# Optimization experiments

Hardware: AMD Instinct MI355X
Metric: run time of the kernel (lower is better)

The kernel has to match this reference:

```python
import jax, jax.numpy as jnp
import numpy as np

D_MODEL = 1024
N_HEADS = 16
N_MEM = 64
D_K = D_MODEL // N_HEADS


def setup_inputs() -> dict:
    key = jax.random.key(0)
    ks = jax.random.split(key, 16)
    B, N = 2, 2048
    s = 1.0 / np.sqrt(D_MODEL)  # xavier-ish scale
    inp = {
        "q": jax.random.normal(ks[0], (B, N, D_MODEL), jnp.float32),
        "k": jax.random.normal(ks[1], (B, N, D_MODEL), jnp.float32),
        "v": jax.random.normal(ks[2], (B, N, D_MODEL), jnp.float32),
        "attention_mask": jax.random.randint(ks[3], (B, 1, 1, N), 0, 2).astype(bool),
        "Wq": jax.random.normal(ks[4], (D_MODEL, D_MODEL), jnp.float32) * s,
        "bq": jnp.zeros((D_MODEL,), jnp.float32),
        "Wk": jax.random.normal(ks[5], (D_MODEL, D_MODEL), jnp.float32) * s,
        "bk": jnp.zeros((D_MODEL,), jnp.float32),
        "Wv": jax.random.normal(ks[6], (D_MODEL, D_MODEL), jnp.float32) * s,
        "bv": jnp.zeros((D_MODEL,), jnp.float32),
        "Wo": jax.random.normal(ks[7], (D_MODEL, D_MODEL), jnp.float32) * s,
        "bo": jnp.zeros((D_MODEL,), jnp.float32),
        "m_k": jax.random.normal(ks[8], (1, N_MEM, D_MODEL), jnp.float32) * 0.01,
        "m_v": jax.random.normal(ks[9], (1, N_MEM, D_MODEL), jnp.float32) * 0.01,
    }
    return inp


def reference(q, k, v, attention_mask, Wq, bq, Wk, bk, Wv, bv, Wo, bo, m_k, m_v):
    B, Nq, D = q.shape
    nk = k.shape[1]
    H, dk, M = N_HEADS, D_K, N_MEM

    # projections (torch Linear: x @ W.T + b)
    qh = (q @ Wq.T + bq).reshape(B, Nq, H, dk).transpose(0, 2, 1, 3)  # b h nq d
    k_proj = k @ Wk.T + bk                                            # b nk d_model
    v_proj = v @ Wv.T + bv

    # append scaled memory slots along key/value length
    mk = jnp.broadcast_to(m_k * np.sqrt(dk), (B, M, D))
    mv = jnp.broadcast_to(m_v * np.sqrt(M), (B, M, D))
    kk = jnp.concatenate([k_proj, mk], axis=1)                        # b (nk+M) d_model
    vv = jnp.concatenate([v_proj, mv], axis=1)

    kh = kk.reshape(B, nk + M, H, dk).transpose(0, 2, 1, 3)          # b h nkM d
    vh = vv.reshape(B, nk + M, H, dk).transpose(0, 2, 1, 3)

    scores = jnp.einsum('bhqd,bhkd->bhqk', qh, kh) / np.sqrt(dk)      # b h nq (nk+M)

    # mask applies only to the first nk key positions; memory slots unmasked
    pad_mask = jnp.concatenate(
        [jnp.broadcast_to(attention_mask, (B, 1, 1, nk)),
         jnp.zeros((B, 1, 1, M), bool)], axis=-1)
    scores = jnp.where(pad_mask, -jnp.inf, scores)

    p_attn = jax.nn.softmax(scores, axis=-1)  # dropout p=0.0 -> identity
    out = jnp.einsum('bhqk,bhkd->bhqd', p_attn, vh)
    out = out.transpose(0, 2, 1, 3).reshape(B, Nq, D)
    return out @ Wo.T + bo
```

## Files before the change

### kernel.cpp

```cpp
#include <hip/hip_runtime.h>
#include <hip/hip_bf16.h>

typedef __attribute__((ext_vector_type(8))) short bf16x8;
typedef __attribute__((ext_vector_type(4))) float f32x4;

__device__ __forceinline__ short f2b(float x) {
    __hip_bfloat16 h = __float2bfloat16(x);
    short s;
    __builtin_memcpy(&s, &h, 2);
    return s;
}

__device__ __forceinline__ void gload16(const short* g, const short* l) {
    __builtin_amdgcn_global_load_lds((const __attribute__((address_space(1))) void*)g,
                                     (__attribute__((address_space(3))) void*)l, 16, 0, 0);
}

__global__ __launch_bounds__(256) void k_prep(const float* __restrict__ q,
                                              const float* __restrict__ k,
                                              const float* __restrict__ v,
                                              const float* __restrict__ Wq,
                                              const float* __restrict__ Wk,
                                              const float* __restrict__ Wv,
                                              const float* __restrict__ Wo,
                                              const float* __restrict__ mk,
                                              const float* __restrict__ mv,
                                              short* __restrict__ dst,
                                              short* __restrict__ kcat,
                                              short* __restrict__ vcat,
                                              short* __restrict__ vt) {
    const int y = blockIdx.y;
    const int i0 = blockIdx.x * 256 + threadIdx.x;
    if (y < 3) {
        const float* src = (y == 0) ? q : (y == 1) ? k : v;
        size_t base = (size_t)y * 1048576;
        #pragma unroll
        for (int it = 0; it < 4; ++it) {
            int off = i0 + it * 262144;
            float4 val = ((const float4*)src)[off];
            short4 o;
            o.x = f2b(val.x); o.y = f2b(val.y); o.z = f2b(val.z); o.w = f2b(val.w);
            ((short4*)dst)[base + off] = o;
        }
    } else if (y < 7) {
        const float* src = (y == 3) ? Wq : (y == 4) ? Wk : (y == 5) ? Wv : Wo;
        size_t base = 3145728 + (size_t)(y - 3) * 262144;
        float4 val = ((const float4*)src)[i0];
        short4 o;
        o.x = f2b(val.x); o.y = f2b(val.y); o.z = f2b(val.z); o.w = f2b(val.w);
        ((short4*)dst)[base + i0] = o;
    } else {
        if (i0 < 131072) {
            int b = i0 >> 16;
            int r = (i0 >> 10) & 63;
            int d = i0 & 1023;
            kcat[((size_t)(b * 2176 + 2048 + r)) * 1024 + d] = f2b(mk[r * 1024 + d] * 8.0f);
            vcat[((size_t)(b * 2176 + 2048 + r)) * 1024 + d] = f2b(mv[r * 1024 + d] * 8.0f);
            kcat[((size_t)(b * 2176 + 2112 + r)) * 1024 + d] = 0;
            int h = (i0 >> 12) & 15, dd = (i0 >> 6) & 63, c = i0 & 63;
            vt[((size_t)((b * 16 + h) * 64 + dd)) * 2176 + 2112 + c] = 0;
        }
    }
}

template <int MODE>
__device__ __forceinline__ void gemm_core(const short* __restrict__ A,
                                          const short* __restrict__ Bw,
                                          const float* __restrict__ bias,
                                          void* __restrict__ Cout,
                                          int bm, int bn,
                                          short (*As)[32], short (*Bs)[32]) {
    const int tid = threadIdx.x;
    const int w = tid >> 6, lane = tid & 63;
    const int wm = w >> 1, wn = w & 1;
    const int lr = lane & 15, lg = lane >> 4;
    const int rseg = lane >> 2;
    const int c_src = (lane & 3) ^ ((lane >> 3) & 3);
    const int slot = lg ^ ((lr >> 1) & 3);

    const short* Ab = A + (size_t)(bm * 128) * 1024;
    const short* Bb = Bw + (size_t)(bn * 128) * 1024;

    f32x4 acc[4][4] = {};

    for (int k0 = 0; k0 < 1024; k0 += 32) {
        __syncthreads();
        #pragma unroll
        for (int jj = 0; jj < 2; ++jj) {
            int seg = w * 2 + jj;
            int row = seg * 16 + rseg;
            gload16(Ab + (size_t)row * 1024 + k0 + c_src * 8, &As[seg * 16][0]);
            gload16(Bb + (size_t)row * 1024 + k0 + c_src * 8, &Bs[seg * 16][0]);
        }
        __syncthreads();
        bf16x8 af[4], bfr[4];
        #pragma unroll
        for (int m = 0; m < 4; ++m) {
            int row = wm * 64 + m * 16 + lr;
            af[m] = *(const bf16x8*)((const char*)As + row * 64 + slot * 16);
        }
        #pragma unroll
        for (int n = 0; n < 4; ++n) {
            int row = wn * 64 + n * 16 + lr;
            bfr[n] = *(const bf16x8*)((const char*)Bs + row * 64 + slot * 16);
        }
        #pragma unroll
        for (int m = 0; m < 4; ++m)
            #pragma unroll
            for (int n = 0; n < 4; ++n)
                acc[m][n] = __builtin_amdgcn_mfma_f32_16x16x32_bf16(af[m], bfr[n], acc[m][n], 0, 0, 0);
    }

    #pragma unroll
    for (int m = 0; m < 4; ++m) {
        #pragma unroll
        for (int n = 0; n < 4; ++n) {
            int col = bn * 128 + wn * 64 + n * 16 + lr;
            float bv = bias[col];
            #pragma unroll
            for (int r = 0; r < 4; ++r) {
                int row = bm * 128 + wm * 64 + m * 16 + lg * 4 + r;
                float val = acc[m][n][r] + bv;
                if (MODE == 0) {
                    ((short*)Cout)[(size_t)row * 1024 + col] = f2b(val);
                } else if (MODE == 1) {
                    int rr = (row >> 11) * 2176 + (row & 2047);
                    ((short*)Cout)[(size_t)rr * 1024 + col] = f2b(val);
                } else {
                    ((float*)Cout)[(size_t)row * 1024 + col] = val;
                }
            }
        }
    }
}

__global__ __launch_bounds__(256) void k_gemm_qkv(const short* __restrict__ qb,
                                                  const short* __restrict__ kb,
                                                  const short* __restrict__ vb,
                                                  const short* __restrict__ Wqb,
                                                  const short* __restrict__ Wkb,
                                                  const short* __restrict__ Wvb,
                                                  const float* __restrict__ bq,
                                                  const float* __restrict__ bk,
                                                  const float* __restrict__ bv,
                                                  short* __restrict__ qp,
                                                  short* __restrict__ kcat,
                                                  short* __restrict__ vcat) {
    __shared__ __align__(16) short As[128][32];
    __shared__ __align__(16) short Bs[128][32];
    const int z = blockIdx.z;
    if (z == 0)      gemm_core<0>(qb, Wqb, bq, qp,   blockIdx.x, blockIdx.y, As, Bs);
    else if (z == 1) gemm_core<1>(kb, Wkb, bk, kcat, blockIdx.x, blockIdx.y, As, Bs);
    else             gemm_core<1>(vb, Wvb, bv, vcat, blockIdx.x, blockIdx.y, As, Bs);
}

__global__ __launch_bounds__(256) void k_gemm_o(const short* __restrict__ aout,
                                                const short* __restrict__ Wob,
                                                const float* __restrict__ bo,
                                                float* __restrict__ out) {
    __shared__ __align__(16) short As[128][32];
    __shared__ __align__(16) short Bs[128][32];
    gemm_core<2>(aout, Wob, bo, out, blockIdx.x, blockIdx.y, As, Bs);
}

__global__ __launch_bounds__(256) void k_vtrans(const short* __restrict__ vcat,
                                                short* __restrict__ vt) {
    __shared__ __align__(16) short t[64][72];
    const int kk0 = blockIdx.x * 64, h = blockIdx.y, b = blockIdx.z;
    const int tid = threadIdx.x;
    const int r = tid >> 3, c = tid & 7;
    #pragma unroll
    for (int i = 0; i < 2; ++i) {
        int row = r + i * 32;
        bf16x8 v = *(const bf16x8*)(vcat + ((size_t)(b * 2176 + kk0 + row)) * 1024 + h * 64 + c * 8);
        *(bf16x8*)(&t[row][c * 8]) = v;
    }
    __syncthreads();
    #pragma unroll
    for (int i = 0; i < 2; ++i) {
        int d = r + i * 32;
        bf16x8 outv;
        #pragma unroll
        for (int j = 0; j < 8; ++j) outv[j] = t[c * 8 + j][d];
        *(bf16x8*)(vt + ((size_t)((b * 16 + h) * 64 + d)) * 2176 + kk0 + c * 8) = outv;
    }
}

__global__ __launch_bounds__(256) void k_attn(const short* __restrict__ qp,
                                              const short* __restrict__ kcat,
                                              const short* __restrict__ vt,
                                              const int* __restrict__ maskI,
                                              short* __restrict__ aout) {
    __shared__ __align__(16) short Ks[2][64][64];
    __shared__ __align__(16) short Vs[2][64][64];
    __shared__ __align__(16) short Pt[4][32][72];
    __shared__ float smask[2176];

    const int bid = blockIdx.x;
    const int x = bid & 7, j = bid >> 3;
    const int g = x + 8 * (j & 3);
    const int qt = j >> 2;
    const int h = g & 15, b = g >> 4;

    const int tid = threadIdx.x;
    const int w = tid >> 6, lane = tid & 63;
    const int lr = lane & 15, lg = lane >> 4;

    for (int i = tid; i < 2176; i += 256) {
        float mval;
        if (i < 2048) mval = maskI[b * 2048 + i] ? -INFINITY : 0.0f;
        else          mval = 0.0f;
        smask[i] = mval;
    }

    const short* Kb = kcat + (size_t)b * 2176 * 1024 + h * 64;
    const short* Vb = vt + ((size_t)(b * 16 + h) * 64) * 2176;

    const int srow8 = lane >> 3;
    const int schunk = (lane & 7) ^ srow8;

    #pragma unroll
    for (int jj = 0; jj < 2; ++jj) {
        int seg = w * 2 + jj;
        int row = seg * 8 + srow8;
        gload16(Kb + (size_t)row * 1024 + schunk * 8, &Ks[0][seg * 8][0]);
        gload16(Vb + (size_t)row * 2176 + schunk * 8, &Vs[0][seg * 8][0]);
    }

    const size_t qbase = ((size_t)(b * 2048 + qt * 128 + w * 32)) * 1024 + h * 64;
    bf16x8 qf[2][2];
    #pragma unroll
    for (int m = 0; m < 2; ++m)
        #pragma unroll
        for (int ks = 0; ks < 2; ++ks)
            qf[m][ks] = *(const bf16x8*)(qp + qbase + (size_t)(m * 16 + lr) * 1024 + ks * 32 + lg * 8);

    float m_run[2][4], l_part[2][4];
    f32x4 o[2][4] = {};
    #pragma unroll
    for (int m = 0; m < 2; ++m)
        #pragma unroll
        for (int r = 0; r < 4; ++r) { m_run[m][r] = -1e30f; l_part[m][r] = 0.0f; }

    __syncthreads();

    int cur = 0;
    for (int t = 0; t < 33; ++t) {
        const int key0 = t * 64;

        if (t < 32) {
            const int nk0 = key0 + 64;
            #pragma unroll
            for (int jj = 0; jj < 2; ++jj) {
                int seg = w * 2 + jj;
                int row = seg * 8 + srow8;
                gload16(Kb + (size_t)(nk0 + row) * 1024 + schunk * 8, &Ks[cur ^ 1][seg * 8][0]);
                gload16(Vb + (size_t)row * 2176 + nk0 + schunk * 8, &Vs[cur ^ 1][seg * 8][0]);
            }
        }

        f32x4 s[2][4] = {};
        #pragma unroll
        for (int ks = 0; ks < 2; ++ks)
            #pragma unroll
            for (int n = 0; n < 4; ++n) {
                int krow = n * 16 + lr;
                int kchunk = (ks * 4 + lg) ^ (lr & 7);
                bf16x8 kf = *(const bf16x8*)((const char*)(&Ks[cur][0][0]) + krow * 128 + kchunk * 16);
                s[0][n] = __builtin_amdgcn_mfma_f32_16x16x32_bf16(qf[0][ks], kf, s[0][n], 0, 0, 0);
                s[1][n] = __builtin_amdgcn_mfma_f32_16x16x32_bf16(qf[1][ks], kf, s[1][n], 0, 0, 0);
            }

        float madd[4];
        #pragma unroll
        for (int n = 0; n < 4; ++n) madd[n] = smask[key0 + n * 16 + lr];

        float lmax[2][4];
        float dmax = -1e30f;
        #pragma unroll
        for (int m = 0; m < 2; ++m)
            #pragma unroll
            for (int r = 0; r < 4; ++r) {
                float a0 = s[m][0][r] * 0.125f + madd[0];
                float a1 = s[m][1][r] * 0.125f + madd[1];
                float a2 = s[m][2][r] * 0.125f + madd[2];
                float a3 = s[m][3][r] * 0.125f + madd[3];
                s[m][0][r] = a0; s[m][1][r] = a1; s[m][2][r] = a2; s[m][3][r] = a3;
                float lm = fmaxf(fmaxf(a0, a1), fmaxf(a2, a3));
                lmax[m][r] = lm;
                dmax = fmaxf(dmax, lm - m_run[m][r]);
            }

        if (__any(dmax > 3.0f)) {
            #pragma unroll
            for (int m = 0; m < 2; ++m)
                #pragma unroll
                for (int r = 0; r < 4; ++r) {
                    float tm = lmax[m][r];
                    #pragma unroll
                    for (int off = 1; off < 16; off <<= 1) tm = fmaxf(tm, __shfl_xor(tm, off));
                    float mnew = fmaxf(m_run[m][r], tm);
                    float corr = __expf(m_run[m][r] - mnew);
                    m_run[m][r] = mnew;
                    l_part[m][r] *= corr;
                    #pragma unroll
                    for (int nO = 0; nO < 4; ++nO) o[m][nO][r] *= corr;
                }
        }

        #pragma unroll
        for (int m = 0; m < 2; ++m)
            #pragma unroll
            for (int n = 0; n < 4; ++n)
                #pragma unroll
                for (int r = 0; r < 4; ++r) {
                    float p = __expf(s[m][n][r] - m_run[m][r]);
                    l_part[m][r] += p;
                    Pt[w][m * 16 + lg * 4 + r][n * 16 + lr] = f2b(p);
                }

        #pragma unroll
        for (int ks2 = 0; ks2 < 2; ++ks2) {
            bf16x8 pa[2];
            pa[0] = *(const bf16x8*)(&Pt[w][lr][ks2 * 32 + lg * 8]);
            pa[1] = *(const bf16x8*)(&Pt[w][16 + lr][ks2 * 32 + lg * 8]);
            #pragma unroll
            for (int nO = 0; nO < 4; ++nO) {
                int vrow = nO * 16 + lr;
                int vchunk = (ks2 * 4 + lg) ^ (lr & 7);
                bf16x8 vf = *(const bf16x8*)((const char*)(&Vs[cur][0][0]) + vrow * 128 + vchunk * 16);
                o[0][nO] = __builtin_amdgcn_mfma_f32_16x16x32_bf16(pa[0], vf, o[0][nO], 0, 0, 0);
                o[1][nO] = __builtin_amdgcn_mfma_f32_16x16x32_bf16(pa[1], vf, o[1][nO], 0, 0, 0);
            }
        }

        __syncthreads();
        cur ^= 1;
    }

    #pragma unroll
    for (int m = 0; m < 2; ++m) {
        #pragma unroll
        for (int r = 0; r < 4; ++r) {
            float l = l_part[m][r];
            #pragma unroll
            for (int off = 1; off < 16; off <<= 1) l += __shfl_xor(l, off);
            float inv = 1.0f / l;
            int qrow = qt * 128 + w * 32 + m * 16 + lg * 4 + r;
            #pragma unroll
            for (int nO = 0; nO < 4; ++nO)
                aout[((size_t)(b * 2048 + qrow)) * 1024 + h * 64 + nO * 16 + lr] =
                    f2b(o[m][nO][r] * inv);
        }
    }
}

extern "C" void kernel_launch(void* const* d_in, const int* in_sizes, int n_in,
                              void* d_out, int out_size, void* d_ws, size_t ws_size,
                              hipStream_t stream) {
    const float* q  = (const float*)d_in[0];
    const float* k  = (const float*)d_in[1];
    const float* v  = (const float*)d_in[2];
    const int* mask = (const int*)d_in[3];
    const float* Wq = (const float*)d_in[4];
    const float* bq = (const float*)d_in[5];
    const float* Wk = (const float*)d_in[6];
    const float* bk = (const float*)d_in[7];
    const float* Wv = (const float*)d_in[8];
    const float* bv = (const float*)d_in[9];
    const float* Wo = (const float*)d_in[10];
    const float* bo = (const float*)d_in[11];
    const float* mk = (const float*)d_in[12];
    const float* mv = (const float*)d_in[13];

    char* ws = (char*)d_ws;
    size_t off = 0;
    auto alloc = [&](size_t bytes) {
        char* p = ws + off;
        off += (bytes + 255) & ~(size_t)255;
        return p;
    };
    short* qb   = (short*)alloc(4096ull * 1024 * 2);
    short* kb   = (short*)alloc(4096ull * 1024 * 2);
    short* vb   = (short*)alloc(4096ull * 1024 * 2);
    short* Wqb  = (short*)alloc(1024ull * 1024 * 2);
    short* Wkb  = (short*)alloc(1024ull * 1024 * 2);
    short* Wvb  = (short*)alloc(1024ull * 1024 * 2);
    short* Wob  = (short*)alloc(1024ull * 1024 * 2);
    short* qp   = (short*)alloc(4096ull * 1024 * 2);
    short* kcat = (short*)alloc(2ull * 2176 * 1024 * 2);
    short* vcat = (short*)alloc(2ull * 2176 * 1024 * 2);
    short* vtb  = (short*)alloc(2ull * 16 * 64 * 2176 * 2);
    short* aout = (short*)alloc(4096ull * 1024 * 2);

    k_prep<<<dim3(1024, 8), 256, 0, stream>>>(q, k, v, Wq, Wk, Wv, Wo, mk, mv,
                                              qb, kcat, vcat, vtb);

    k_gemm_qkv<<<dim3(32, 8, 3), 256, 0, stream>>>(qb, kb, vb, Wqb, Wkb, Wvb,
                                                   bq, bk, bv, qp, kcat, vcat);

    k_vtrans<<<dim3(33, 16, 2), 256, 0, stream>>>(vcat, vtb);

    k_attn<<<512, 256, 0, stream>>>(qp, kcat, vtb, mask, aout);

    k_gemm_o<<<dim3(32, 8), 256, 0, stream>>>(aout, Wob, bo, (float*)d_out);
}
```

Before: 153.6 us.

## Use 8 waves of 16 query rows and transposed S=K·Q MFMA layout in attention

Doubles the attention block to 512 threads so each wave handles 16 query rows instead of 32. The score MFMA operands are swapped so each lane holds one query column, which removes the 16-lane max and sum shuffle reductions and vectorizes the mask load. P is written to LDS as packed pairs, and an explicit lgkmcnt wait is added before P is read back. This halves per-wave register pressure and should raise parallelism, but each K/V tile is now amortized over fewer rows per wave and the per-row correction needs extra lane shuffles.

```diff
diff --git a/kernel.cpp b/kernel.cpp
--- a/kernel.cpp
+++ b/kernel.cpp
@@ -186,14 +186,14 @@
     }
 }
 
-__global__ __launch_bounds__(256) void k_attn(const short* __restrict__ qp,
+__global__ __launch_bounds__(512) void k_attn(const short* __restrict__ qp,
                                               const short* __restrict__ kcat,
                                               const short* __restrict__ vt,
                                               const int* __restrict__ maskI,
                                               short* __restrict__ aout) {
     __shared__ __align__(16) short Ks[2][64][64];
     __shared__ __align__(16) short Vs[2][64][64];
-    __shared__ __align__(16) short Pt[4][32][72];
+    __shared__ __align__(16) short Pt[8][16][72];
     __shared__ float smask[2176];
 
     const int bid = blockIdx.x;
@@ -206,7 +206,7 @@
     const int w = tid >> 6, lane = tid & 63;
     const int lr = lane & 15, lg = lane >> 4;
 
-    for (int i = tid; i < 2176; i += 256) {
+    for (int i = tid; i < 2176; i += 512) {
         float mval;
         if (i < 2048) mval = maskI[b * 2048 + i] ? -INFINITY : 0.0f;
         else          mval = 0.0f;
@@ -219,28 +219,20 @@
     const int srow8 = lane >> 3;
     const int schunk = (lane & 7) ^ srow8;
 
-    #pragma unroll
-    for (int jj = 0; jj < 2; ++jj) {
-        int seg = w * 2 + jj;
-        int row = seg * 8 + srow8;
-        gload16(Kb + (size_t)row * 1024 + schunk * 8, &Ks[0][seg * 8][0]);
-        gload16(Vb + (size_t)row * 2176 + schunk * 8, &Vs[0][seg * 8][0]);
-    }
-
-    const size_t qbase = ((size_t)(b * 2048 + qt * 128 + w * 32)) * 1024 + h * 64;
-    bf16x8 qf[2][2];
-    #pragma unroll
-    for (int m = 0; m < 2; ++m)
-        #pragma unroll
-        for (int ks = 0; ks < 2; ++ks)
-            qf[m][ks] = *(const bf16x8*)(qp + qbase + (size_t)(m * 16 + lr) * 1024 + ks * 32 + lg * 8);
-
-    float m_run[2][4], l_part[2][4];
-    f32x4 o[2][4] = {};
-    #pragma unroll
-    for (int m = 0; m < 2; ++m)
-        #pragma unroll
-        for (int r = 0; r < 4; ++r) { m_run[m][r] = -1e30f; l_part[m][r] = 0.0f; }
+    {
+        int row = w * 8 + srow8;
+        gload16(Kb + (size_t)row * 1024 + schunk * 8, &Ks[0][w * 8][0]);
+        gload16(Vb + (size_t)row * 2176 + schunk * 8, &Vs[0][w * 8][0]);
+    }
+
+    const size_t qbase = ((size_t)(b * 2048 + qt * 128 + w * 16)) * 1024 + h * 64;
+    bf16x8 qf[2];
+    #pragma unroll
+    for (int ks = 0; ks < 2; ++ks)
+        qf[ks] = *(const bf16x8*)(qp + qbase + (size_t)lr * 1024 + ks * 32 + lg * 8);
+
+    float m_run = -1e30f, l_part = 0.0f;
+    f32x4 o[4] = {};
 
     __syncthreads();
 
@@ -250,16 +242,12 @@
 
         if (t < 32) {
             const int nk0 = key0 + 64;
-            #pragma unroll
-            for (int jj = 0; jj < 2; ++jj) {
-                int seg = w * 2 + jj;
-                int row = seg * 8 + srow8;
-                gload16(Kb + (size_t)(nk0 + row) * 1024 + schunk * 8, &Ks[cur ^ 1][seg * 8][0]);
-                gload16(Vb + (size_t)row * 2176 + nk0 + schunk * 8, &Vs[cur ^ 1][seg * 8][0]);
-            }
-        }
-
-        f32x4 s[2][4] = {};
+            int row = w * 8 + srow8;
+            gload16(Kb + (size_t)(nk0 + row) * 1024 + schunk * 8, &Ks[cur ^ 1][w * 8][0]);
+            gload16(Vb + (size_t)row * 2176 + nk0 + schunk * 8, &Vs[cur ^ 1][w * 8][0]);
+        }
+
+        f32x4 s[4] = {};
         #pragma unroll
         for (int ks = 0; ks < 2; ++ks)
             #pragma unroll
@@ -267,70 +255,62 @@
                 int krow = n * 16 + lr;
                 int kchunk = (ks * 4 + lg) ^ (lr & 7);
                 bf16x8 kf = *(const bf16x8*)((const char*)(&Ks[cur][0][0]) + krow * 128 + kchunk * 16);
-                s[0][n] = __builtin_amdgcn_mfma_f32_16x16x32_bf16(qf[0][ks], kf, s[0][n], 0, 0, 0);
-                s[1][n] = __builtin_amdgcn_mfma_f32_16x16x32_bf16(qf[1][ks], kf, s[1][n], 0, 0, 0);
+                s[n] = __builtin_amdgcn_mfma_f32_16x16x32_bf16(kf, qf[ks], s[n], 0, 0, 0);
             }
 
-        float madd[4];
-        #pragma unroll
-        for (int n = 0; n < 4; ++n) madd[n] = smask[key0 + n * 16 + lr];
-
-        float lmax[2][4];
-        float dmax = -1e30f;
-        #pragma unroll
-        for (int m = 0; m < 2; ++m)
+        float lm = -1e30f;
+        #pragma unroll
+        for (int n = 0; n < 4; ++n) {
+            float4 mq = *(const float4*)(&smask[key0 + n * 16 + lg * 4]);
+            s[n][0] = s[n][0] * 0.125f + mq.x;
+            s[n][1] = s[n][1] * 0.125f + mq.y;
+            s[n][2] = s[n][2] * 0.125f + mq.z;
+            s[n][3] = s[n][3] * 0.125f + mq.w;
+            lm = fmaxf(lm, fmaxf(fmaxf(s[n][0], s[n][1]), fmaxf(s[n][2], s[n][3])));
+        }
+
+        if (__any(lm - m_run > 3.0f)) {
+            float tm = lm;
+            tm = fmaxf(tm, __shfl_xor(tm, 16));
+            tm = fmaxf(tm, __shfl_xor(tm, 32));
+            float mnew = fmaxf(m_run, tm);
+            float corr = __expf(m_run - mnew);
+            m_run = mnew;
+            l_part *= corr;
             #pragma unroll
             for (int r = 0; r < 4; ++r) {
-                float a0 = s[m][0][r] * 0.125f + madd[0];
-                float a1 = s[m][1][r] * 0.125f + madd[1];
-                float a2 = s[m][2][r] * 0.125f + madd[2];
-                float a3 = s[m][3][r] * 0.125f + madd[3];
-                s[m][0][r] = a0; s[m][1][r] = a1; s[m][2][r] = a2; s[m][3][r] = a3;
-                float lm = fmaxf(fmaxf(a0, a1), fmaxf(a2, a3));
-                lmax[m][r] = lm;
-                dmax = fmaxf(dmax, lm - m_run[m][r]);
+                float cb = __shfl(corr, 20 * lg + r);
+                #pragma unroll
+                for (int nO = 0; nO < 4; ++nO) o[nO][r] *= cb;
             }
-
-        if (__any(dmax > 3.0f)) {
-            #pragma unroll
-            for (int m = 0; m < 2; ++m)
-                #pragma unroll
-                for (int r = 0; r < 4; ++r) {
-                    float tm = lmax[m][r];
-                    #pragma unroll
-                    for (int off = 1; off < 16; off <<= 1) tm = fmaxf(tm, __shfl_xor(tm, off));
-                    float mnew = fmaxf(m_run[m][r], tm);
-                    float corr = __expf(m_run[m][r] - mnew);
-                    m_run[m][r] = mnew;
-                    l_part[m][r] *= corr;
-                    #pragma unroll
-                    for (int nO = 0; nO < 4; ++nO) o[m][nO][r] *= corr;
-                }
-        }
-
-        #pragma unroll
-        for (int m = 0; m < 2; ++m)
-            #pragma unroll
-            for (int n = 0; n < 4; ++n)
-                #pragma unroll
-                for (int r = 0; r < 4; ++r) {
-                    float p = __expf(s[m][n][r] - m_run[m][r]);
-                    l_part[m][r] += p;
-                    Pt[w][m * 16 + lg * 4 + r][n * 16 + lr] = f2b(p);
-                }
+        }
+
+        #pragma unroll
+        for (int n = 0; n < 4; ++n) {
+            float p0 = __expf(s[n][0] - m_run);
+            float p1 = __expf(s[n][1] - m_run);
+            float p2 = __expf(s[n][2] - m_run);
+            float p3 = __expf(s[n][3] - m_run);
+            l_part += (p0 + p1) + (p2 + p3);
+            unsigned pk[2];
+            pk[0] = (unsigned)(unsigned short)f2b(p0) | ((unsigned)(unsigned short)f2b(p1) << 16);
+            pk[1] = (unsigned)(unsigned short)f2b(p2) | ((unsigned)(unsigned short)f2b(p3) << 16);
+            __builtin_memcpy((char*)(&Pt[w][0][0]) + lr * 144 + n * 32 + lg * 8, pk, 8);
+        }
+
+        asm volatile("s_waitcnt lgkmcnt(0)" ::: "memory");
+        __builtin_amdgcn_sched_barrier(0);
 
         #pragma unroll
         for (int ks2 = 0; ks2 < 2; ++ks2) {
-            bf16x8 pa[2];
-            pa[0] = *(const bf16x8*)(&Pt[w][lr][ks2 * 32 + lg * 8]);
-            pa[1] = *(const bf16x8*)(&Pt[w][16 + lr][ks2 * 32 + lg * 8]);
+            bf16x8 pa;
+            __builtin_memcpy(&pa, (const char*)(&Pt[w][0][0]) + lr * 144 + ks2 * 64 + lg * 16, 16);
             #pragma unroll
             for (int nO = 0; nO < 4; ++nO) {
                 int vrow = nO * 16 + lr;
                 int vchunk = (ks2 * 4 + lg) ^ (lr & 7);
                 bf16x8 vf = *(const bf16x8*)((const char*)(&Vs[cur][0][0]) + vrow * 128 + vchunk * 16);
-                o[0][nO] = __builtin_amdgcn_mfma_f32_16x16x32_bf16(pa[0], vf, o[0][nO], 0, 0, 0);
-                o[1][nO] = __builtin_amdgcn_mfma_f32_16x16x32_bf16(pa[1], vf, o[1][nO], 0, 0, 0);
+                o[nO] = __builtin_amdgcn_mfma_f32_16x16x32_bf16(pa, vf, o[nO], 0, 0, 0);
             }
         }
 
@@ -338,20 +318,18 @@
         cur ^= 1;
     }
 
-    #pragma unroll
-    for (int m = 0; m < 2; ++m) {
-        #pragma unroll
-        for (int r = 0; r < 4; ++r) {
-            float l = l_part[m][r];
-            #pragma unroll
-            for (int off = 1; off < 16; off <<= 1) l += __shfl_xor(l, off);
-            float inv = 1.0f / l;
-            int qrow = qt * 128 + w * 32 + m * 16 + lg * 4 + r;
-            #pragma unroll
-            for (int nO = 0; nO < 4; ++nO)
-                aout[((size_t)(b * 2048 + qrow)) * 1024 + h * 64 + nO * 16 + lr] =
-                    f2b(o[m][nO][r] * inv);
-        }
+    float l = l_part;
+    l += __shfl_xor(l, 16);
+    l += __shfl_xor(l, 32);
+    float inv = 1.0f / l;
+    #pragma unroll
+    for (int r = 0; r < 4; ++r) {
+        float ib = __shfl(inv, 20 * lg + r);
+        int qrow = qt * 128 + w * 16 + lg * 4 + r;
+        #pragma unroll
+        for (int nO = 0; nO < 4; ++nO)
+            aout[((size_t)(b * 2048 + qrow)) * 1024 + h * 64 + nO * 16 + lr] =
+                f2b(o[nO][r] * ib);
     }
 }
 
@@ -401,7 +379,7 @@
 
     k_vtrans<<<dim3(33, 16, 2), 256, 0, stream>>>(vcat, vtb);
 
-    k_attn<<<512, 256, 0, stream>>>(qp, kcat, vtb, mask, aout);
+    k_attn<<<512, 512, 0, stream>>>(qp, kcat, vtb, mask, aout);
 
     k_gemm_o<<<dim3(32, 8), 256, 0, stream>>>(aout, Wob, bo, (float*)d_out);
 }
```

Measured after the change: 141.4 us. 7.9% less time.
